# Optimization experiments

Hardware: AMD Instinct MI355X
Metric: run time of the kernel (lower is better)

Reference implementation:

```python
import jax, jax.numpy as jnp
import numpy as np

FEATURE_DIM = 1024
HEADS = 16
HEAD_DIM = FEATURE_DIM // HEADS


def setup_inputs() -> dict:
    key = jax.random.key(0)
    ks = jax.random.split(key, 9)
    B, C, T = 4, FEATURE_DIM, 4096
    s = 1.0 / np.sqrt(C)
    inp = {
        "x": jax.random.normal(ks[0], (B, C, T), dtype=jnp.float32),
        "Wq": jax.random.uniform(ks[1], (C, C), jnp.float32, -s, s),
        "bq": jax.random.uniform(ks[2], (C,), jnp.float32, -s, s),
        "Wk": jax.random.uniform(ks[3], (C, C), jnp.float32, -s, s),
        "bk": jax.random.uniform(ks[4], (C,), jnp.float32, -s, s),
        "Wv": jax.random.uniform(ks[5], (C, C), jnp.float32, -s, s),
        "bv": jax.random.uniform(ks[6], (C,), jnp.float32, -s, s),
        "Wo": jax.random.uniform(ks[7], (C, C), jnp.float32, -s, s),
        "bo": jax.random.uniform(ks[8], (C,), jnp.float32, -s, s),
    }
    return inp


def reference(x, Wq, bq, Wk, bk, Wv, bv, Wo, bo):
    B, C, T = x.shape
    H, D = HEADS, HEAD_DIM
    xt = jnp.transpose(x, (0, 2, 1))  # [B, T, C]
    # torch Linear: y = x @ W.T + b
    q = jax.nn.elu(xt @ Wq.T + bq).reshape(B, T, H, D) + 1.0
    k = jax.nn.elu(xt @ Wk.T + bk).reshape(B, T, H, D) + 1.0
    v = (xt @ Wv.T + bv).reshape(B, T, H, D)
    kv = jnp.einsum('bthd,bthe->bhde', k, v)      # [B, H, D, D]
    z = jnp.einsum('bthd,bhd->bth', q, k.sum(axis=1))  # [B, T, H]
    num = jnp.einsum('bthd,bhde->bthe', q, kv)    # [B, T, H, D]
    out = num / (z[..., None] + 1e-6)
    out = out.reshape(B, T, C)
    out = out @ Wo.T + bo  # dropout is identity in eval mode
    return jnp.transpose(out + xt, (0, 2, 1))  # [B, C, T]
```

## Files before the change

kernel.cpp:

```cpp
#include <hip/hip_runtime.h>
#include <hip/hip_bf16.h>
#include <cmath>

typedef unsigned short u16;
typedef unsigned int   u32;

#define BB 4
#define CC 1024
#define TT 4096
#define HH 16
#define DD 64

using bf16x8 = __attribute__((ext_vector_type(8))) __bf16;
using f32x4  = __attribute__((ext_vector_type(4))) float;

union FragU { bf16x8 v; u16 u[8]; };

__device__ __forceinline__ float bf2f(u16 u) {
    union { u32 i; float f; } v; v.i = ((u32)u) << 16; return v.f;
}
__device__ __forceinline__ u16 f2bf(float f) {
    union { float f; u32 i; } v; v.f = f;
    u32 x = v.i;
    return (u16)((x + 0x7fffu + ((x >> 16) & 1u)) >> 16);
}

__device__ __forceinline__ void gl_lds16(const u16* g, u16* l) {
    __builtin_amdgcn_global_load_lds(
        (const __attribute__((address_space(1))) void*)g,
        (__attribute__((address_space(3))) void*)l, 16, 0, 0);
}

__global__ __launch_bounds__(256) void prep_kernel(
    const float* __restrict__ x,
    const float* __restrict__ Wq, const float* __restrict__ Wk,
    const float* __restrict__ Wv, const float* __restrict__ Wo,
    u16* __restrict__ xt, u16* __restrict__ Wcat, u16* __restrict__ Wob,
    float* __restrict__ kvz)
{
    __shared__ u16 tile[64 * 258];
    const int id  = blockIdx.x;
    const int tid = threadIdx.x;

    if (id < 1024) {
        const int t0 = (id & 63) * 64;
        const int c0 = ((id >> 6) & 3) * 256;
        const int b  = id >> 8;
        const float* xb  = x  + (size_t)b * CC * TT;
        u16*         xtb = xt + (size_t)b * TT * CC;
        const int tcol = tid & 63;
        const int rw   = tid >> 6;
        #pragma unroll 8
        for (int p = 0; p < 64; ++p) {
            const int cr = p * 4 + rw;
            tile[tcol * 258 + cr] = f2bf(xb[(size_t)(c0 + cr) * TT + t0 + tcol]);
        }
        __syncthreads();
        const int cp = tid & 127;
        const int th = tid >> 7;
        #pragma unroll 8
        for (int q = 0; q < 32; ++q) {
            const int tr = q * 2 + th;
            const u32 v = *reinterpret_cast<const u32*>(&tile[tr * 258 + cp * 2]);
            *reinterpret_cast<u32*>(&xtb[(size_t)(t0 + tr) * CC + c0 + cp * 2]) = v;
        }
    } else if (id < 5120) {
        const int id2  = id - 1024;
        const int wsel = id2 >> 10;
        const int i    = ((id2 & 1023) * 256 + tid) * 4;
        const float* src = (wsel == 0) ? Wq : (wsel == 1) ? Wk : (wsel == 2) ? Wv : Wo;
        u16* dst = (wsel < 3) ? (Wcat + (size_t)wsel * CC * CC) : Wob;
        const float4 v = *reinterpret_cast<const float4*>(src + i);
        ushort4 o;
        o.x = f2bf(v.x); o.y = f2bf(v.y); o.z = f2bf(v.z); o.w = f2bf(v.w);
        *reinterpret_cast<ushort4*>(dst + i) = o;
    } else {
        const int idx = ((id - 5120) * 256 + tid) * 4;
        *reinterpret_cast<float4*>(&kvz[idx]) = (float4){0.f, 0.f, 0.f, 0.f};
    }
}

__global__ __launch_bounds__(256, 2) void kvfuse_kernel(
    const u16* __restrict__ A, const u16* __restrict__ Wk,
    const u16* __restrict__ Wv, const float* __restrict__ bk,
    const float* __restrict__ bv, float* __restrict__ kv,
    float* __restrict__ ksum)
{
    __shared__ __align__(16) char smem[49152];
    u16* As  = (u16*)smem;
    u16* WKs = (u16*)(smem + 16384);
    u16* WVs = (u16*)(smem + 32768);

    const int tid  = threadIdx.x;
    const int w    = tid >> 6;
    const int lane = tid & 63;
    const int wm = w >> 1, wn = w & 1;
    const int quad = lane >> 4, l16 = lane & 15;

    const int bid = blockIdx.x;
    const int sw  = (bid & 7) * 128 + (bid >> 3);
    const int n0  = (sw & 7) * 128;
    const int m0  = (sw >> 3) * 128;

    const int srow = lane >> 3;
    const int scol = ((lane & 7) ^ srow) * 8;

    f32x4 ak[4][4], av[4][4];
    #pragma unroll
    for (int i = 0; i < 4; ++i)
        #pragma unroll
        for (int j = 0; j < 4; ++j) { ak[i][j] = (f32x4)0.0f; av[i][j] = (f32x4)0.0f; }

    for (int k0 = 0; k0 < CC; k0 += 64) {
        __syncthreads();
        #pragma unroll
        for (int s = 0; s < 4; ++s) {
            gl_lds16(A  + (size_t)(m0 + 32 * w + 8 * s + srow) * CC + k0 + scol,
                     &As [(32 * w + 8 * s) * 64]);
            gl_lds16(Wk + (size_t)(n0 + 32 * w + 8 * s + srow) * CC + k0 + scol,
                     &WKs[(32 * w + 8 * s) * 64]);
            gl_lds16(Wv + (size_t)(n0 + 32 * w + 8 * s + srow) * CC + k0 + scol,
                     &WVs[(32 * w + 8 * s) * 64]);
        }
        __syncthreads();

        #pragma unroll
        for (int sub = 0; sub < 2; ++sub) {
            const int pg = (((sub << 2) | quad) ^ (l16 & 7)) * 8;
            bf16x8 af[4], bk4[4], bv4[4];
            #pragma unroll
            for (int i = 0; i < 4; ++i) {
                af[i]  = *reinterpret_cast<const bf16x8*>(&As [(wm * 64 + i * 16 + l16) * 64 + pg]);
                bk4[i] = *reinterpret_cast<const bf16x8*>(&WKs[(wn * 64 + i * 16 + l16) * 64 + pg]);
                bv4[i] = *reinterpret_cast<const bf16x8*>(&WVs[(wn * 64 + i * 16 + l16) * 64 + pg]);
            }
            #pragma unroll
            for (int i = 0; i < 4; ++i)
                #pragma unroll
                for (int j = 0; j < 4; ++j) {
                    ak[i][j] = __builtin_amdgcn_mfma_f32_16x16x32_bf16(af[i], bk4[j], ak[i][j], 0, 0, 0);
                    av[i][j] = __builtin_amdgcn_mfma_f32_16x16x32_bf16(af[i], bv4[j], av[i][j], 0, 0, 0);
                }
        }
    }

    u16* Kl = (u16*)smem;
    u16* Vl = (u16*)(smem + 16384);

    float bkk[4], bvv[4];
    #pragma unroll
    for (int j = 0; j < 4; ++j) {
        bkk[j] = bk[n0 + wn * 64 + j * 16 + l16];
        bvv[j] = bv[n0 + wn * 64 + j * 16 + l16];
    }

    const int hh    = w >> 1;
    const int dbase = (w & 1) * 32;
    const int b     = m0 >> 12;
    const int bh    = b * HH + (sw & 7) * 2 + hh;

    FragU ones;
    #pragma unroll
    for (int j = 0; j < 8; ++j) ones.u[j] = (l16 == 0) ? 0x3F80u : 0u;

    f32x4 ckv[2][4], cks[2];
    #pragma unroll
    for (int s = 0; s < 2; ++s) {
        cks[s] = (f32x4)0.0f;
        #pragma unroll
        for (int e4 = 0; e4 < 4; ++e4) ckv[s][e4] = (f32x4)0.0f;
    }

    #pragma unroll
    for (int h = 0; h < 2; ++h) {
        __syncthreads();
        if (wm == h) {
            #pragma unroll
            for (int i = 0; i < 4; ++i) {
                const int t6 = i * 16 + quad * 4;
                #pragma unroll
                for (int j = 0; j < 4; ++j) {
                    const int c    = wn * 64 + j * 16 + l16;
                    const int toff = t6 ^ ((c & 7) * 8);
                    ushort4 oK, oV;
                    #pragma unroll
                    for (int r = 0; r < 4; ++r) {
                        float vK = ak[i][j][r] + bkk[j];
                        vK = (vK > 0.0f) ? (vK + 1.0f) : __expf(vK);
                        ((u16*)&oK)[r] = f2bf(vK);
                        ((u16*)&oV)[r] = f2bf(av[i][j][r] + bvv[j]);
                    }
                    *reinterpret_cast<ushort4*>(&Kl[c * 64 + toff]) = oK;
                    *reinterpret_cast<ushort4*>(&Vl[c * 64 + toff]) = oV;
                }
            }
        }
        __syncthreads();
        #pragma unroll
        for (int kt = 0; kt < 2; ++kt) {
            const int tg = kt * 32 + quad * 8;
            #pragma unroll
            for (int s = 0; s < 2; ++s) {
                const int ca = hh * 64 + dbase + s * 16 + l16;
                const bf16x8 af = *reinterpret_cast<const bf16x8*>(
                    &Kl[ca * 64 + (tg ^ ((ca & 7) * 8))]);
                #pragma unroll
                for (int e4 = 0; e4 < 4; ++e4) {
                    const int cb = hh * 64 + e4 * 16 + l16;
                    const bf16x8 bfv = *reinterpret_cast<const bf16x8*>(
                        &Vl[cb * 64 + (tg ^ ((cb & 7) * 8))]);
                    ckv[s][e4] = __builtin_amdgcn_mfma_f32_16x16x32_bf16(af, bfv, ckv[s][e4], 0, 0, 0);
                }
                cks[s] = __builtin_amdgcn_mfma_f32_16x16x32_bf16(af, ones.v, cks[s], 0, 0, 0);
            }
        }
    }

    float* kvb = kv + (size_t)bh * DD * DD;
    #pragma unroll
    for (int s = 0; s < 2; ++s)
        #pragma unroll
        for (int e4 = 0; e4 < 4; ++e4)
            #pragma unroll
            for (int r = 0; r < 4; ++r)
                atomicAdd(&kvb[(dbase + s * 16 + quad * 4 + r) * DD + e4 * 16 + l16],
                          ckv[s][e4][r]);
    if (l16 == 0) {
        #pragma unroll
        for (int s = 0; s < 2; ++s)
            #pragma unroll
            for (int r = 0; r < 4; ++r)
                atomicAdd(&ksum[bh * DD + dbase + s * 16 + quad * 4 + r], cks[s][r]);
    }
}

__global__ __launch_bounds__(256, 2) void qattn_kernel(
    const u16* __restrict__ A, const u16* __restrict__ Wq,
    const float* __restrict__ bq, const float* __restrict__ kv,
    const float* __restrict__ ksum, u16* __restrict__ attnO)
{
    __shared__ __align__(16) char smem[32768];
    u16* As = (u16*)smem;
    u16* Ws = (u16*)(smem + 16384);

    const int tid  = threadIdx.x;
    const int w    = tid >> 6;
    const int lane = tid & 63;
    const int wm = w >> 1, wn = w & 1;
    const int quad = lane >> 4, l16 = lane & 15;
    const int l7 = l16 & 7;

    const int bid = blockIdx.x;
    const int sw  = (bid & 7) * 128 + (bid >> 3);
    const int n0  = (sw & 7) * 128;
    const int m0  = (sw >> 3) * 128;

    const int srow = lane >> 3;
    const int scol = ((lane & 7) ^ srow) * 8;

    f32x4 acc[4][4];
    #pragma unroll
    for (int i = 0; i < 4; ++i)
        #pragma unroll
        for (int j = 0; j < 4; ++j) acc[i][j] = (f32x4)0.0f;

    for (int k0 = 0; k0 < CC; k0 += 64) {
        __syncthreads();
        #pragma unroll
        for (int s = 0; s < 4; ++s) {
            gl_lds16(A  + (size_t)(m0 + 32 * w + 8 * s + srow) * CC + k0 + scol,
                     &As[(32 * w + 8 * s) * 64]);
            gl_lds16(Wq + (size_t)(n0 + 32 * w + 8 * s + srow) * CC + k0 + scol,
                     &Ws[(32 * w + 8 * s) * 64]);
        }
        __syncthreads();

        #pragma unroll
        for (int sub = 0; sub < 2; ++sub) {
            const int pg = (((sub << 2) | quad) ^ l7) * 8;
            bf16x8 af[4], bfr[4];
            #pragma unroll
            for (int i = 0; i < 4; ++i) {
                af[i]  = *reinterpret_cast<const bf16x8*>(&As[(wm * 64 + i * 16 + l16) * 64 + pg]);
                bfr[i] = *reinterpret_cast<const bf16x8*>(&Ws[(wn * 64 + i * 16 + l16) * 64 + pg]);
            }
            #pragma unroll
            for (int i = 0; i < 4; ++i)
                #pragma unroll
                for (int j = 0; j < 4; ++j)
                    acc[i][j] = __builtin_amdgcn_mfma_f32_16x16x32_bf16(af[i], bfr[j], acc[i][j], 0, 0, 0);
        }
    }

    __syncthreads();
    u16* Qt = (u16*)smem;
    float bqq[4];
    #pragma unroll
    for (int j = 0; j < 4; ++j) bqq[j] = bq[n0 + wn * 64 + j * 16 + l16];
    #pragma unroll
    for (int i = 0; i < 4; ++i) {
        #pragma unroll
        for (int j = 0; j < 4; ++j) {
            const int c = wn * 64 + j * 16 + l16;
            #pragma unroll
            for (int r = 0; r < 4; ++r) {
                const int t = wm * 64 + i * 16 + quad * 4 + r;
                float v = acc[i][j][r] + bqq[j];
                v = (v > 0.0f) ? (v + 1.0f) : __expf(v);
                Qt[t * 128 + (c ^ ((t & 7) * 8))] = f2bf(v);
            }
        }
    }
    __syncthreads();

    const int hh = w >> 1, th = w & 1;
    const int b  = m0 >> 12;
    const int bh = b * HH + (sw & 7) * 2 + hh;
    const float* kvh = kv + (size_t)bh * DD * DD;

    FragU bf[4][2], zb[2];
    #pragma unroll
    for (int ck = 0; ck < 2; ++ck) {
        #pragma unroll
        for (int nt = 0; nt < 4; ++nt)
            #pragma unroll
            for (int j = 0; j < 8; ++j)
                bf[nt][ck].u[j] = f2bf(kvh[(ck * 32 + quad * 8 + j) * DD + nt * 16 + l16]);
        #pragma unroll
        for (int j = 0; j < 8; ++j)
            zb[ck].u[j] = (l16 == 0) ? f2bf(ksum[bh * DD + ck * 32 + quad * 8 + j]) : 0u;
    }

    f32x4 a2[4][4], za[4];
    #pragma unroll
    for (int i = 0; i < 4; ++i) {
        za[i] = (f32x4)0.0f;
        #pragma unroll
        for (int j = 0; j < 4; ++j) a2[i][j] = (f32x4)0.0f;
    }

    #pragma unroll
    for (int i = 0; i < 4; ++i) {
        const int trow = th * 64 + i * 16 + l16;
        #pragma unroll
        for (int ck = 0; ck < 2; ++ck) {
            const bf16x8 af = *reinterpret_cast<const bf16x8*>(
                &Qt[trow * 128 + (((hh * 8 + ck * 4 + quad) ^ l7) * 8)]);
            #pragma unroll
            for (int nt = 0; nt < 4; ++nt)
                a2[i][nt] = __builtin_amdgcn_mfma_f32_16x16x32_bf16(af, bf[nt][ck].v, a2[i][nt], 0, 0, 0);
            za[i] = __builtin_amdgcn_mfma_f32_16x16x32_bf16(af, zb[ck].v, za[i], 0, 0, 0);
        }
    }

    #pragma unroll
    for (int i = 0; i < 4; ++i) {
        float inv[4];
        #pragma unroll
        for (int r = 0; r < 4; ++r) {
            const float zv = __shfl(za[i][r], lane & 48);
            inv[r] = 1.0f / (zv + 1e-6f);
        }
        #pragma unroll
        for (int nt = 0; nt < 4; ++nt) {
            #pragma unroll
            for (int r = 0; r < 4; ++r) {
                const size_t row = (size_t)(m0 + th * 64 + i * 16 + quad * 4 + r);
                const int    col = n0 + hh * 64 + nt * 16 + l16;
                attnO[row * CC + col] = f2bf(a2[i][nt][r] * inv[r]);
            }
        }
    }
}

template <int MODE>
__global__ __launch_bounds__(256, 2) void gemm_kernel(
    const u16* __restrict__ A, const u16* __restrict__ W,
    const float* __restrict__ b0, const float* __restrict__ b1,
    const float* __restrict__ b2, u16* __restrict__ Ybf,
    float* __restrict__ Yf, const float* __restrict__ xres,
    int M, int N, int K)
{
    __shared__ char smem[34048];
    u16* As = (u16*)smem;
    u16* Ws = (u16*)(smem + 16384);

    const int tid  = threadIdx.x;
    const int w    = tid >> 6;
    const int lane = tid & 63;
    const int wm = w >> 1, wn = w & 1;
    const int quad = lane >> 4, l16 = lane & 15;

    const int bid = blockIdx.x;
    const int sw  = (bid & 7) * 128 + (bid >> 3);
    const int n0  = (sw & 7) * 128;
    const int m0  = (sw >> 3) * 128;

    const int srow = lane >> 3;
    const int scol = ((lane & 7) ^ srow) * 8;

    f32x4 acc[4][4];
    #pragma unroll
    for (int i = 0; i < 4; ++i)
        #pragma unroll
        for (int j = 0; j < 4; ++j) acc[i][j] = (f32x4)0.0f;

    for (int k0 = 0; k0 < K; k0 += 64) {
        __syncthreads();
        #pragma unroll
        for (int s = 0; s < 4; ++s)
            gl_lds16(A + (size_t)(m0 + 32 * w + 8 * s + srow) * K + k0 + scol,
                     &As[(32 * w + 8 * s) * 64]);
        #pragma unroll
        for (int s = 0; s < 4; ++s)
            gl_lds16(W + (size_t)(n0 + 32 * w + 8 * s + srow) * K + k0 + scol,
                     &Ws[(32 * w + 8 * s) * 64]);
        __syncthreads();

        #pragma unroll
        for (int sub = 0; sub < 2; ++sub) {
            const int pg = (((sub << 2) | quad) ^ (l16 & 7)) * 8;
            bf16x8 af[4], bfr[4];
            #pragma unroll
            for (int i = 0; i < 4; ++i) {
                af[i]  = *reinterpret_cast<const bf16x8*>(&As[(wm * 64 + i * 16 + l16) * 64 + pg]);
                bfr[i] = *reinterpret_cast<const bf16x8*>(&Ws[(wn * 64 + i * 16 + l16) * 64 + pg]);
            }
            #pragma unroll
            for (int i = 0; i < 4; ++i)
                #pragma unroll
                for (int j = 0; j < 4; ++j)
                    acc[i][j] = __builtin_amdgcn_mfma_f32_16x16x32_bf16(af[i], bfr[j], acc[i][j], 0, 0, 0);
        }
    }

    if (MODE == 2) {
        float* Cs = (float*)smem;
        const int b     = m0 / TT;
        const int tbase = m0 - b * TT;
        const int cl    = lane >> 4;
        #pragma unroll
        for (int hh = 0; hh < 2; ++hh) {
            __syncthreads();
            if (wm == hh) {
                #pragma unroll
                for (int i = 0; i < 4; ++i)
                    #pragma unroll
                    for (int j = 0; j < 4; ++j)
                        #pragma unroll
                        for (int r = 0; r < 4; ++r)
                            Cs[(i * 16 + quad * 4 + r) * 133 + wn * 64 + j * 16 + l16] = acc[i][j][r];
            }
            __syncthreads();
            #pragma unroll
            for (int p = 0; p < 8; ++p) {
                const int col = p * 16 + w * 4 + cl;
                const int tl  = l16 * 4;
                float4 v;
                v.x = Cs[(tl + 0) * 133 + col];
                v.y = Cs[(tl + 1) * 133 + col];
                v.z = Cs[(tl + 2) * 133 + col];
                v.w = Cs[(tl + 3) * 133 + col];
                const float bv = b0[n0 + col];
                const size_t base = ((size_t)b * CC + n0 + col) * TT + tbase + hh * 64 + tl;
                const float4 rx = *reinterpret_cast<const float4*>(&xres[base]);
                v.x += bv + rx.x; v.y += bv + rx.y;
                v.z += bv + rx.z; v.w += bv + rx.w;
                *reinterpret_cast<float4*>(&Yf[base]) = v;
            }
        }
    }
}

extern "C" void kernel_launch(void* const* d_in, const int* in_sizes, int n_in,
                              void* d_out, int out_size, void* d_ws, size_t ws_size,
                              hipStream_t stream)
{
    const float* x  = (const float*)d_in[0];
    const float* Wq = (const float*)d_in[1];
    const float* bq = (const float*)d_in[2];
    const float* Wk = (const float*)d_in[3];
    const float* bk = (const float*)d_in[4];
    const float* Wv = (const float*)d_in[5];
    const float* bv = (const float*)d_in[6];
    const float* Wo = (const float*)d_in[7];
    const float* bo = (const float*)d_in[8];
    float* out = (float*)d_out;

    const int M = BB * TT;
    const size_t BUF  = (size_t)BB * TT * CC * sizeof(u16);
    const size_t WBUF = (size_t)CC * CC * sizeof(u16);

    char* ws = (char*)d_ws;
    u16* xt   = (u16*)(ws);
    u16* Qb   = (u16*)(ws + BUF);
    u16* Wcat = (u16*)(ws + 4 * BUF);
    u16* Wob  = (u16*)(ws + 4 * BUF + 3 * WBUF);
    float* kvbuf = (float*)(ws + 4 * BUF + 4 * WBUF);
    float* ksumb = kvbuf + (size_t)BB * HH * DD * DD;

    prep_kernel<<<5380, 256, 0, stream>>>(x, Wq, Wk, Wv, Wo, xt, Wcat, Wob, kvbuf);

    kvfuse_kernel<<<1024, 256, 0, stream>>>(
        xt, Wcat + (size_t)CC * CC, Wcat + 2 * (size_t)CC * CC, bk, bv, kvbuf, ksumb);

    qattn_kernel<<<1024, 256, 0, stream>>>(
        xt, Wcat, bq, kvbuf, ksumb, Qb);

    gemm_kernel<2><<<1024, 256, 0, stream>>>(
        Qb, Wob, bo, nullptr, nullptr, nullptr, out, x, M, CC, CC);
}
```

Baseline: 322.3 us.

## Process two M tiles per kvfuse block and vectorize x transpose loads

The kvfuse kernel now handles two 128-row M tiles per block, with half as many blocks. It accumulates kv/ksum across both tiles in registers, which halves the atomicAdd traffic. The K/V staging buffers get their own LDS region so the first k-slice of the next tile can be prefetched during the epilogue. The prep transpose now reads x with float4 loads instead of scalar loads. The cost is more LDS per block (80KB), which may cut occupancy, and fewer blocks for the GPU to spread across its CUs.

```diff
diff --git a/kernel.cpp b/kernel.cpp
--- a/kernel.cpp
+++ b/kernel.cpp
@@ -48,12 +48,17 @@
         const int b  = id >> 8;
         const float* xb  = x  + (size_t)b * CC * TT;
         u16*         xtb = xt + (size_t)b * TT * CC;
-        const int tcol = tid & 63;
-        const int rw   = tid >> 6;
-        #pragma unroll 8
-        for (int p = 0; p < 64; ++p) {
-            const int cr = p * 4 + rw;
-            tile[tcol * 258 + cr] = f2bf(xb[(size_t)(c0 + cr) * TT + t0 + tcol]);
+        const int t4 = (tid & 15) * 4;
+        const int cl = tid >> 4;
+        #pragma unroll
+        for (int q = 0; q < 16; ++q) {
+            const int cr = q * 16 + cl;
+            const float4 v = *reinterpret_cast<const float4*>(
+                &xb[(size_t)(c0 + cr) * TT + t0 + t4]);
+            tile[(t4 + 0) * 258 + cr] = f2bf(v.x);
+            tile[(t4 + 1) * 258 + cr] = f2bf(v.y);
+            tile[(t4 + 2) * 258 + cr] = f2bf(v.z);
+            tile[(t4 + 3) * 258 + cr] = f2bf(v.w);
         }
         __syncthreads();
         const int cp = tid & 127;
@@ -86,10 +91,12 @@
     const float* __restrict__ bv, float* __restrict__ kv,
     float* __restrict__ ksum)
 {
-    __shared__ __align__(16) char smem[49152];
+    __shared__ __align__(16) char smem[81920];
     u16* As  = (u16*)smem;
     u16* WKs = (u16*)(smem + 16384);
     u16* WVs = (u16*)(smem + 32768);
+    u16* Kl  = (u16*)(smem + 49152);
+    u16* Vl  = (u16*)(smem + 65536);
 
     const int tid  = threadIdx.x;
     const int w    = tid >> 6;
@@ -98,54 +105,17 @@
     const int quad = lane >> 4, l16 = lane & 15;
 
     const int bid = blockIdx.x;
-    const int sw  = (bid & 7) * 128 + (bid >> 3);
+    const int sw  = (bid & 7) * 64 + (bid >> 3);
     const int n0  = (sw & 7) * 128;
-    const int m0  = (sw >> 3) * 128;
+    const int mb  = (sw >> 3) * 256;
 
     const int srow = lane >> 3;
     const int scol = ((lane & 7) ^ srow) * 8;
 
-    f32x4 ak[4][4], av[4][4];
-    #pragma unroll
-    for (int i = 0; i < 4; ++i)
-        #pragma unroll
-        for (int j = 0; j < 4; ++j) { ak[i][j] = (f32x4)0.0f; av[i][j] = (f32x4)0.0f; }
-
-    for (int k0 = 0; k0 < CC; k0 += 64) {
-        __syncthreads();
-        #pragma unroll
-        for (int s = 0; s < 4; ++s) {
-            gl_lds16(A  + (size_t)(m0 + 32 * w + 8 * s + srow) * CC + k0 + scol,
-                     &As [(32 * w + 8 * s) * 64]);
-            gl_lds16(Wk + (size_t)(n0 + 32 * w + 8 * s + srow) * CC + k0 + scol,
-                     &WKs[(32 * w + 8 * s) * 64]);
-            gl_lds16(Wv + (size_t)(n0 + 32 * w + 8 * s + srow) * CC + k0 + scol,
-                     &WVs[(32 * w + 8 * s) * 64]);
-        }
-        __syncthreads();
-
-        #pragma unroll
-        for (int sub = 0; sub < 2; ++sub) {
-            const int pg = (((sub << 2) | quad) ^ (l16 & 7)) * 8;
-            bf16x8 af[4], bk4[4], bv4[4];
-            #pragma unroll
-            for (int i = 0; i < 4; ++i) {
-                af[i]  = *reinterpret_cast<const bf16x8*>(&As [(wm * 64 + i * 16 + l16) * 64 + pg]);
-                bk4[i] = *reinterpret_cast<const bf16x8*>(&WKs[(wn * 64 + i * 16 + l16) * 64 + pg]);
-                bv4[i] = *reinterpret_cast<const bf16x8*>(&WVs[(wn * 64 + i * 16 + l16) * 64 + pg]);
-            }
-            #pragma unroll
-            for (int i = 0; i < 4; ++i)
-                #pragma unroll
-                for (int j = 0; j < 4; ++j) {
-                    ak[i][j] = __builtin_amdgcn_mfma_f32_16x16x32_bf16(af[i], bk4[j], ak[i][j], 0, 0, 0);
-                    av[i][j] = __builtin_amdgcn_mfma_f32_16x16x32_bf16(af[i], bv4[j], av[i][j], 0, 0, 0);
-                }
-        }
-    }
-
-    u16* Kl = (u16*)smem;
-    u16* Vl = (u16*)(smem + 16384);
+    const int hh    = w >> 1;
+    const int dbase = (w & 1) * 32;
+    const int b     = mb >> 12;
+    const int bh    = b * HH + (sw & 7) * 2 + hh;
 
     float bkk[4], bvv[4];
     #pragma unroll
@@ -154,11 +124,6 @@
         bvv[j] = bv[n0 + wn * 64 + j * 16 + l16];
     }
 
-    const int hh    = w >> 1;
-    const int dbase = (w & 1) * 32;
-    const int b     = m0 >> 12;
-    const int bh    = b * HH + (sw & 7) * 2 + hh;
-
     FragU ones;
     #pragma unroll
     for (int j = 0; j < 8; ++j) ones.u[j] = (l16 == 0) ? 0x3F80u : 0u;
@@ -171,50 +136,108 @@
         for (int e4 = 0; e4 < 4; ++e4) ckv[s][e4] = (f32x4)0.0f;
     }
 
-    #pragma unroll
-    for (int h = 0; h < 2; ++h) {
+#define STAGE(M0, K0)                                                               \
+    { _Pragma("unroll")                                                             \
+      for (int s_ = 0; s_ < 4; ++s_) {                                              \
+        gl_lds16(A  + (size_t)((M0) + 32 * w + 8 * s_ + srow) * CC + (K0) * 64 + scol, \
+                 &As [(32 * w + 8 * s_) * 64]);                                     \
+        gl_lds16(Wk + (size_t)(n0 + 32 * w + 8 * s_ + srow) * CC + (K0) * 64 + scol,   \
+                 &WKs[(32 * w + 8 * s_) * 64]);                                     \
+        gl_lds16(Wv + (size_t)(n0 + 32 * w + 8 * s_ + srow) * CC + (K0) * 64 + scol,   \
+                 &WVs[(32 * w + 8 * s_) * 64]); } }
+
+#define BARL() { asm volatile("s_waitcnt lgkmcnt(0)" ::: "memory"); \
+                 __builtin_amdgcn_s_barrier();                      \
+                 asm volatile("" ::: "memory"); }
+
+    STAGE(mb, 0);
+
+    for (int mt = 0; mt < 2; ++mt) {
+        const int m0 = mb + mt * 128;
+
+        f32x4 ak[4][4], av[4][4];
+        #pragma unroll
+        for (int i = 0; i < 4; ++i)
+            #pragma unroll
+            for (int j = 0; j < 4; ++j) { ak[i][j] = (f32x4)0.0f; av[i][j] = (f32x4)0.0f; }
+
+        for (int ks = 0; ks < 16; ++ks) {
+            if (ks > 0) {
+                __syncthreads();
+                STAGE(m0, ks);
+            }
+            __syncthreads();
+
+            #pragma unroll
+            for (int sub = 0; sub < 2; ++sub) {
+                const int pg = (((sub << 2) | quad) ^ (l16 & 7)) * 8;
+                bf16x8 af[4], bk4[4], bv4[4];
+                #pragma unroll
+                for (int i = 0; i < 4; ++i) {
+                    af[i]  = *reinterpret_cast<const bf16x8*>(&As [(wm * 64 + i * 16 + l16) * 64 + pg]);
+                    bk4[i] = *reinterpret_cast<const bf16x8*>(&WKs[(wn * 64 + i * 16 + l16) * 64 + pg]);
+                    bv4[i] = *reinterpret_cast<const bf16x8*>(&WVs[(wn * 64 + i * 16 + l16) * 64 + pg]);
+                }
+                #pragma unroll
+                for (int i = 0; i < 4; ++i)
+                    #pragma unroll
+                    for (int j = 0; j < 4; ++j) {
+                        ak[i][j] = __builtin_amdgcn_mfma_f32_16x16x32_bf16(af[i], bk4[j], ak[i][j], 0, 0, 0);
+                        av[i][j] = __builtin_amdgcn_mfma_f32_16x16x32_bf16(af[i], bv4[j], av[i][j], 0, 0, 0);
+                    }
+            }
+        }
+
         __syncthreads();
-        if (wm == h) {
-            #pragma unroll
-            for (int i = 0; i < 4; ++i) {
-                const int t6 = i * 16 + quad * 4;
-                #pragma unroll
-                for (int j = 0; j < 4; ++j) {
-                    const int c    = wn * 64 + j * 16 + l16;
-                    const int toff = t6 ^ ((c & 7) * 8);
-                    ushort4 oK, oV;
+        if (mt == 0) STAGE(mb + 128, 0);
+
+        #pragma unroll
+        for (int h = 0; h < 2; ++h) {
+            BARL();
+            if (wm == h) {
+                #pragma unroll
+                for (int i = 0; i < 4; ++i) {
+                    const int t6 = i * 16 + quad * 4;
                     #pragma unroll
-                    for (int r = 0; r < 4; ++r) {
-                        float vK = ak[i][j][r] + bkk[j];
-                        vK = (vK > 0.0f) ? (vK + 1.0f) : __expf(vK);
-                        ((u16*)&oK)[r] = f2bf(vK);
-                        ((u16*)&oV)[r] = f2bf(av[i][j][r] + bvv[j]);
+                    for (int j = 0; j < 4; ++j) {
+                        const int c    = wn * 64 + j * 16 + l16;
+                        const int toff = t6 ^ ((c & 7) * 8);
+                        ushort4 oK, oV;
+                        #pragma unroll
+                        for (int r = 0; r < 4; ++r) {
+                            float vK = ak[i][j][r] + bkk[j];
+                            vK = (vK > 0.0f) ? (vK + 1.0f) : __expf(vK);
+                            ((u16*)&oK)[r] = f2bf(vK);
+                            ((u16*)&oV)[r] = f2bf(av[i][j][r] + bvv[j]);
+                        }
+                        *reinterpret_cast<ushort4*>(&Kl[c * 64 + toff]) = oK;
+                        *reinterpret_cast<ushort4*>(&Vl[c * 64 + toff]) = oV;
                     }
-                    *reinterpret_cast<ushort4*>(&Kl[c * 64 + toff]) = oK;
-                    *reinterpret_cast<ushort4*>(&Vl[c * 64 + toff]) = oV;
                 }
             }
-        }
-        __syncthreads();
-        #pragma unroll
-        for (int kt = 0; kt < 2; ++kt) {
-            const int tg = kt * 32 + quad * 8;
-            #pragma unroll
-            for (int s = 0; s < 2; ++s) {
-                const int ca = hh * 64 + dbase + s * 16 + l16;
-                const bf16x8 af = *reinterpret_cast<const bf16x8*>(
-                    &Kl[ca * 64 + (tg ^ ((ca & 7) * 8))]);
-                #pragma unroll
-                for (int e4 = 0; e4 < 4; ++e4) {
-                    const int cb = hh * 64 + e4 * 16 + l16;
-                    const bf16x8 bfv = *reinterpret_cast<const bf16x8*>(
-                        &Vl[cb * 64 + (tg ^ ((cb & 7) * 8))]);
-                    ckv[s][e4] = __builtin_amdgcn_mfma_f32_16x16x32_bf16(af, bfv, ckv[s][e4], 0, 0, 0);
+            BARL();
+            #pragma unroll
+            for (int kt = 0; kt < 2; ++kt) {
+                const int tg = kt * 32 + quad * 8;
+                #pragma unroll
+                for (int s = 0; s < 2; ++s) {
+                    const int ca = hh * 64 + dbase + s * 16 + l16;
+                    const bf16x8 af = *reinterpret_cast<const bf16x8*>(
+                        &Kl[ca * 64 + (tg ^ ((ca & 7) * 8))]);
+                    #pragma unroll
+                    for (int e4 = 0; e4 < 4; ++e4) {
+                        const int cb = hh * 64 + e4 * 16 + l16;
+                        const bf16x8 bfv = *reinterpret_cast<const bf16x8*>(
+                            &Vl[cb * 64 + (tg ^ ((cb & 7) * 8))]);
+                        ckv[s][e4] = __builtin_amdgcn_mfma_f32_16x16x32_bf16(af, bfv, ckv[s][e4], 0, 0, 0);
+                    }
+                    cks[s] = __builtin_amdgcn_mfma_f32_16x16x32_bf16(af, ones.v, cks[s], 0, 0, 0);
                 }
-                cks[s] = __builtin_amdgcn_mfma_f32_16x16x32_bf16(af, ones.v, cks[s], 0, 0, 0);
-            }
-        }
-    }
+            }
+        }
+    }
+#undef BARL
+#undef STAGE
 
     float* kvb = kv + (size_t)bh * DD * DD;
     #pragma unroll
@@ -501,7 +524,7 @@
 
     prep_kernel<<<5380, 256, 0, stream>>>(x, Wq, Wk, Wv, Wo, xt, Wcat, Wob, kvbuf);
 
-    kvfuse_kernel<<<1024, 256, 0, stream>>>(
+    kvfuse_kernel<<<512, 256, 0, stream>>>(
         xt, Wcat + (size_t)CC * CC, Wcat + 2 * (size_t)CC * CC, bk, bv, kvbuf, ksumb);
 
     qattn_kernel<<<1024, 256, 0, stream>>>(
```

Result: slower. 345.4 us (+7.2%).
